# Kernel tuning notes

Measured on AMD Instinct MI355X. Metric: run time of the kernel, lower is better.

The kernel has to match this reference:

```python
import jax, jax.numpy as jnp
import numpy as np

B, S, F_IN, D, DFF, MEM, L, H = 32, 512, 64, 512, 2048, 1024, 3, 8
K_NEIGH = 3
TEMP = 1.0


def _pos_encoding(s, d):
    pos = np.arange(s, dtype=np.float64)[:, None]
    div = np.exp(np.arange(0, d, 2, dtype=np.float64) * (-np.log(10000.0) / d))
    pe = np.zeros((s, d), np.float32)
    pe[:, 0::2] = np.sin(pos * div)
    pe[:, 1::2] = np.cos(pos * div)
    return jnp.asarray(pe)


def _ln(x, g, b, eps=1e-5):
    m = x.mean(-1, keepdims=True)
    v = ((x - m) ** 2).mean(-1, keepdims=True)
    return (x - m) * jax.lax.rsqrt(v + eps) * g + b


def _mha(x, qkv_w, qkv_b, out_w, out_b):
    b, s, d = x.shape
    dh = d // H
    qkv = x @ qkv_w.T + qkv_b                      # (b,s,3d)
    q, k, v = jnp.split(qkv, 3, axis=-1)
    rs = lambda t: t.reshape(b, s, H, dh).transpose(0, 2, 1, 3)   # (b,h,s,dh)
    q, k, v = rs(q), rs(k), rs(v)
    scores = jnp.einsum('bhqd,bhkd->bhqk', q, k) / np.sqrt(dh).astype(np.float32)
    att = jax.nn.softmax(scores, axis=-1)
    o = jnp.einsum('bhqk,bhkd->bhqd', att, v).transpose(0, 2, 1, 3).reshape(b, s, d)
    return o @ out_w.T + out_b


def _construct_graph(x):
    # x: (B, S, F) -> adjacency (B, F, F) via kNN on rank-1 similarity (as in source)
    f = x.mean(axis=1)                                   # (B,F)
    n = jnp.linalg.norm(f, axis=1, keepdims=True)
    fn = f / jnp.maximum(n, 1e-12)                       # F.normalize over full vector
    sim = jnp.einsum('bi,bj->bij', fn, fn)               # (B,F,F)
    nf = f.shape[1]
    k = min(K_NEIGH, nf - 1)
    _, idx = jax.lax.top_k(sim, k + 1)                   # (B,F,k+1)
    idx = idx[..., 1:]                                   # drop top-1 (self under source's assumption)
    bidx = jnp.arange(f.shape[0])[:, None, None]
    ridx = jnp.arange(nf)[None, :, None]
    A = jnp.zeros((f.shape[0], nf, nf), x.dtype).at[bidx, ridx, idx].set(1.0)
    A = jnp.maximum(A, jnp.swapaxes(A, 1, 2))            # symmetrize
    di = jnp.arange(nf)
    return A.at[:, di, di].set(1.0)                      # fill_diagonal_(1)


def _gcn(x, A, w1, b1, w2, b2):
    deg = A.sum(2, keepdims=True)
    An = A / jnp.where(deg == 0, jnp.ones_like(deg), deg)
    xt = jnp.swapaxes(x, 1, 2)                           # (B,F,S)
    h = jax.nn.relu(jnp.einsum('bfg,bgh->bfh', An, xt @ w1.T + b1))
    h = jnp.einsum('bfg,bgh->bfh', An, h @ w2.T + b2)
    return jnp.swapaxes(h, 1, 2)                         # (B,S,F)


def _metg_forward(x, W_in, b_in, qkv_w, qkv_b, out_w, out_b, ln1_g, ln1_b,
                  ln2_g, ln2_b, ff1_w, ff1_b, ff2_w, ff2_b, memory,
                  fc1_w, fc1_b, fc2_w, fc2_b, gc1_w, gc1_b, gc2_w, gc2_b):
    # transformer branch
    h = x @ W_in.T + b_in                                # (B,S,D)
    h = h + _pos_encoding(h.shape[1], h.shape[2])
    for l in range(L):  # post-norm TransformerEncoderLayer, relu FFN, dropout=eval
        h = _ln(h + _mha(h, qkv_w[l], qkv_b[l], out_w[l], out_b[l]), ln1_g[l], ln1_b[l])
        ff = jax.nn.relu(h @ ff1_w[l].T + ff1_b[l]) @ ff2_w[l].T + ff2_b[l]
        h = _ln(h + ff, ln2_g[l], ln2_b[l])
    # memory module
    sims = (h @ memory.T) / TEMP                         # (B,S,MEM)
    attn = jax.nn.softmax(sims, axis=-1)
    upd = attn @ memory                                  # (B,S,D)
    # decoder
    cat = jnp.concatenate([h, upd], axis=-1)             # (B,S,2D)
    t_out = jax.nn.relu(cat @ fc1_w.T + fc1_b) @ fc2_w.T + fc2_b
    # GCN branch
    A = _construct_graph(x)
    g_out = _gcn(x, A, gc1_w, gc1_b, gc2_w, gc2_b)
    return t_out, g_out, attn


def setup_inputs() -> dict:
    key = jax.random.key(0)
    ks = jax.random.split(key, 12)
    w = lambda k, shape, s=0.02: jax.random.normal(k, shape, jnp.float32) * s
    return {
        'x': jax.random.normal(ks[0], (B, S, F_IN), jnp.float32),
        'W_in': w(ks[1], (D, F_IN)), 'b_in': jnp.zeros((D,), jnp.float32),
        'qkv_w': w(ks[2], (L, 3 * D, D)), 'qkv_b': jnp.zeros((L, 3 * D), jnp.float32),
        'out_w': w(ks[3], (L, D, D)), 'out_b': jnp.zeros((L, D), jnp.float32),
        'ln1_g': jnp.ones((L, D), jnp.float32), 'ln1_b': jnp.zeros((L, D), jnp.float32),
        'ln2_g': jnp.ones((L, D), jnp.float32), 'ln2_b': jnp.zeros((L, D), jnp.float32),
        'ff1_w': w(ks[4], (L, DFF, D)), 'ff1_b': jnp.zeros((L, DFF), jnp.float32),
        'ff2_w': w(ks[5], (L, D, DFF)), 'ff2_b': jnp.zeros((L, D), jnp.float32),
        'memory': w(ks[6], (MEM, D), 0.05),
        'fc1_w': w(ks[7], (D, 2 * D)), 'fc1_b': jnp.zeros((D,), jnp.float32),
        'fc2_w': w(ks[8], (F_IN, D)), 'fc2_b': jnp.zeros((F_IN,), jnp.float32),
        'gc1_w': w(ks[9], (D, S)), 'gc1_b': jnp.zeros((D,), jnp.float32),
        'gc2_w': w(ks[10], (S, D)), 'gc2_b': jnp.zeros((S,), jnp.float32),
    }


def reference(x, W_in, b_in, qkv_w, qkv_b, out_w, out_b, ln1_g, ln1_b,
              ln2_g, ln2_b, ff1_w, ff1_b, ff2_w, ff2_b, memory,
              fc1_w, fc1_b, fc2_w, fc2_b, gc1_w, gc1_b, gc2_w, gc2_b):
    return _metg_forward(x, W_in, b_in, qkv_w, qkv_b, out_w, out_b, ln1_g, ln1_b,
                         ln2_g, ln2_b, ff1_w, ff1_b, ff2_w, ff2_b, memory,
                         fc1_w, fc1_b, fc2_w, fc2_b, gc1_w, gc1_b, gc2_w, gc2_b)
```

## Files before the change

kernel.cpp:

```cpp
#include <hip/hip_runtime.h>
#include <hip/hip_bf16.h>
#include <math.h>


namespace {

typedef unsigned short ushort_t;
using bf16x8 = __attribute__((ext_vector_type(8))) __bf16;
using f32x4 = __attribute__((ext_vector_type(4))) float;
using ushort8 = __attribute__((ext_vector_type(8))) unsigned short;

constexpr int Mrows = 32 * 512;
constexpr size_t MB = 1048576;

__device__ __forceinline__ unsigned short f2bf(float f) {
  unsigned int u = __builtin_bit_cast(unsigned int, f);
  u += 0x7fffu + ((u >> 16) & 1u);
  return (unsigned short)(u >> 16);
}
__device__ __forceinline__ float bf2f(ushort_t u) {
  unsigned int v = ((unsigned int)u) << 16;
  return __builtin_bit_cast(float, v);
}

__device__ __forceinline__ void g2lds16(const void* g, void* l) {
  __builtin_amdgcn_global_load_lds(
      (const __attribute__((address_space(1))) unsigned int*)g,
      (__attribute__((address_space(3))) unsigned int*)l, 16, 0, 0);
}

template <bool RELU, bool BF16OUT>
__global__ __launch_bounds__(256) void gemm_bf16(const ushort_t* __restrict__ A,
                                                 const ushort_t* __restrict__ B,
                                                 const float* __restrict__ bias,
                                                 void* __restrict__ Cv,
                                                 int K, int lda, int ldc, int Nclip) {
  __shared__ __align__(16) ushort_t As[128 * 64];
  __shared__ __align__(16) ushort_t Bs[128 * 64];
  const int t = threadIdx.x;
  const int w = t >> 6, l = t & 63;
  const int m0 = blockIdx.x << 7, n0 = blockIdx.y << 7;
  const int srow8 = l >> 3;
  const int scol = ((l & 7) ^ srow8) << 3;
  const ushort_t* agp = A + (size_t)(m0 + w * 32 + srow8) * lda + scol;
  const ushort_t* bgp = B + (size_t)(n0 + w * 32 + srow8) * K + scol;
  ushort_t* alds = &As[(w * 32) * 64];
  ushort_t* blds = &Bs[(w * 32) * 64];
  const int wr = w >> 1, wc = w & 1;
  const int lr = l & 15, g = l >> 4;
  const int sw = (l & 7) << 4;
  f32x4 acc[4][4] = {};
  for (int kt = 0; kt < K; kt += 64) {
    __syncthreads();
#pragma unroll
    for (int i = 0; i < 4; ++i) {
      g2lds16(agp + (size_t)(i * 8) * lda + kt, alds + i * 8 * 64);
      g2lds16(bgp + (size_t)(i * 8) * K + kt, blds + i * 8 * 64);
    }
    __syncthreads();
#pragma unroll
    for (int ki = 0; ki < 2; ++ki) {
      bf16x8 af[4], bf[4];
      const int kb = (ki * 64 + g * 16) ^ sw;
#pragma unroll
      for (int mi = 0; mi < 4; ++mi)
        af[mi] = *(const bf16x8*)((const char*)As + (wr * 64 + mi * 16 + lr) * 128 + kb);
#pragma unroll
      for (int ni = 0; ni < 4; ++ni)
        bf[ni] = *(const bf16x8*)((const char*)Bs + (wc * 64 + ni * 16 + lr) * 128 + kb);
#pragma unroll
      for (int mi = 0; mi < 4; ++mi)
#pragma unroll
        for (int ni = 0; ni < 4; ++ni)
          acc[mi][ni] = __builtin_amdgcn_mfma_f32_16x16x32_bf16(af[mi], bf[ni],
                                                                acc[mi][ni], 0, 0, 0);
    }
  }
  float bb[4];
#pragma unroll
  for (int ni = 0; ni < 4; ++ni) {
    const int ci = n0 + wc * 64 + ni * 16 + lr;
    bb[ni] = (bias && ci < Nclip) ? bias[ci] : 0.f;
  }
  const int crow0 = m0 + wr * 64 + g * 4;
#pragma unroll
  for (int mi = 0; mi < 4; ++mi)
#pragma unroll
    for (int ni = 0; ni < 4; ++ni) {
      const int ci = n0 + wc * 64 + ni * 16 + lr;
      if (ci >= Nclip) continue;
#pragma unroll
      for (int v = 0; v < 4; ++v) {
        float val = acc[mi][ni][v] + bb[ni];
        if (RELU) val = fmaxf(val, 0.f);
        const size_t off = (size_t)(crow0 + mi * 16 + v) * ldc + ci;
        if (BF16OUT) ((ushort_t*)Cv)[off] = f2bf(val);
        else         ((float*)Cv)[off] = val;
      }
    }
}

__global__ __launch_bounds__(256) void flash_attn_mfma(const ushort_t* __restrict__ qkvb,
                                                       ushort_t* __restrict__ ctxb) {
  __shared__ __align__(16) ushort_t Qs[64 * 64];
  __shared__ __align__(16) ushort_t Ks[64 * 64];
  __shared__ __align__(16) ushort_t VT[64 * 64];
  __shared__ __align__(16) ushort_t Ps[64 * 64];
  const int qb = blockIdx.x, hh = blockIdx.y, b = blockIdx.z;
  const int t = threadIdx.x, w = t >> 6, l = t & 63;
  const int g = l >> 4, lr = l & 15, l7 = l & 7;
  const ushort_t* qkv0 = qkvb + (size_t)b * 512 * 1536 + hh * 64;
  {
    const int r8 = l >> 3;
    const int gcol = (l7 ^ r8) << 3;
#pragma unroll
    for (int i = 0; i < 2; ++i) {
      const int row = w * 16 + i * 8 + r8;
      g2lds16(qkv0 + (size_t)(qb * 64 + row) * 1536 + gcol, &Qs[(w * 16 + i * 8) * 64]);
    }
  }
  float mst = -INFINITY, lst = 0.f;
  f32x4 oacc[4] = {};
  const int vk0 = (t & 31) * 2;
  const int vdh0 = (t >> 5) * 8;
  for (int kt = 0; kt < 8; ++kt) {
    __syncthreads();
    {
      const int r8 = l >> 3;
      const int gcol = (l7 ^ r8) << 3;
#pragma unroll
      for (int i = 0; i < 2; ++i) {
        const int row = w * 16 + i * 8 + r8;
        g2lds16(qkv0 + 512 + (size_t)(kt * 64 + row) * 1536 + gcol,
                &Ks[(w * 16 + i * 8) * 64]);
      }
    }
    {
      const ushort_t* vp = qkv0 + 1024 + (size_t)(kt * 64 + vk0) * 1536 + vdh0;
      ushort8 v0 = *(const ushort8*)vp;
      ushort8 v1 = *(const ushort8*)(vp + 1536);
      const int slotbase = vk0 >> 3;
      const int inb = (vk0 & 7) * 2;
#pragma unroll
      for (int e = 0; e < 8; ++e) {
        const int dh = vdh0 + e;
        unsigned int word = (unsigned int)v0[e] | ((unsigned int)v1[e] << 16);
        *(unsigned int*)((char*)VT + dh * 128 + (((slotbase ^ (dh & 7)) << 4) + inb)) = word;
      }
    }
    __syncthreads();
    f32x4 sacc[4] = {};
#pragma unroll
    for (int ki = 0; ki < 2; ++ki) {
      const int sb = ((ki * 4 + g) ^ l7) << 4;
      bf16x8 qf = *(const bf16x8*)((const char*)Qs + (w * 16 + lr) * 128 + sb);
#pragma unroll
      for (int mi = 0; mi < 4; ++mi) {
        bf16x8 kf = *(const bf16x8*)((const char*)Ks + (mi * 16 + lr) * 128 + sb);
        sacc[mi] = __builtin_amdgcn_mfma_f32_16x16x32_bf16(kf, qf, sacc[mi], 0, 0, 0);
      }
    }
    float p[4][4];
    float cmax = -INFINITY;
#pragma unroll
    for (int mi = 0; mi < 4; ++mi)
#pragma unroll
      for (int v = 0; v < 4; ++v) {
        p[mi][v] = sacc[mi][v] * 0.125f;
        cmax = fmaxf(cmax, p[mi][v]);
      }
    cmax = fmaxf(cmax, __shfl_xor(cmax, 16));
    cmax = fmaxf(cmax, __shfl_xor(cmax, 32));
    const float mnew = fmaxf(mst, cmax);
    const float al = __expf(mst - mnew);
    float csum = 0.f;
#pragma unroll
    for (int mi = 0; mi < 4; ++mi)
#pragma unroll
      for (int v = 0; v < 4; ++v) {
        p[mi][v] = __expf(p[mi][v] - mnew);
        csum += p[mi][v];
      }
    csum += __shfl_xor(csum, 16);
    csum += __shfl_xor(csum, 32);
    lst = lst * al + csum;
    mst = mnew;
#pragma unroll
    for (int mi = 0; mi < 4; ++mi) oacc[mi] *= al;
    {
      char* pbase = (char*)Ps + (w * 16 + lr) * 128;
#pragma unroll
      for (int mi = 0; mi < 4; ++mi)
#pragma unroll
        for (int vp2 = 0; vp2 < 2; ++vp2) {
          const int klo = mi * 16 + g * 4 + vp2 * 2;
          unsigned int word = (unsigned int)f2bf(p[mi][vp2 * 2]) |
                              ((unsigned int)f2bf(p[mi][vp2 * 2 + 1]) << 16);
          *(unsigned int*)(pbase + (((klo >> 3) ^ l7) << 4) + (klo & 7) * 2) = word;
        }
    }
#pragma unroll
    for (int ki = 0; ki < 2; ++ki) {
      const int sb = ((ki * 4 + g) ^ l7) << 4;
      bf16x8 pf = *(const bf16x8*)((const char*)Ps + (w * 16 + lr) * 128 + sb);
#pragma unroll
      for (int mi = 0; mi < 4; ++mi) {
        bf16x8 vf = *(const bf16x8*)((const char*)VT + (mi * 16 + lr) * 128 + sb);
        oacc[mi] = __builtin_amdgcn_mfma_f32_16x16x32_bf16(vf, pf, oacc[mi], 0, 0, 0);
      }
    }
  }
  const float inv = 1.f / lst;
  ushort_t* op = ctxb + (size_t)(b * 512 + qb * 64 + w * 16 + lr) * 512 + hh * 64;
#pragma unroll
  for (int mi = 0; mi < 4; ++mi)
#pragma unroll
    for (int vp2 = 0; vp2 < 2; ++vp2) {
      const int dh = mi * 16 + g * 4 + vp2 * 2;
      unsigned int word = (unsigned int)f2bf(oacc[mi][vp2 * 2] * inv) |
                          ((unsigned int)f2bf(oacc[mi][vp2 * 2 + 1] * inv) << 16);
      *(unsigned int*)(op + dh) = word;
    }
}

#define OUTER16(ACC, A4, B4) do { \
  ACC[0][0] += (A4).x*(B4).x; ACC[0][1] += (A4).x*(B4).y; ACC[0][2] += (A4).x*(B4).z; ACC[0][3] += (A4).x*(B4).w; \
  ACC[1][0] += (A4).y*(B4).x; ACC[1][1] += (A4).y*(B4).y; ACC[1][2] += (A4).y*(B4).z; ACC[1][3] += (A4).y*(B4).w; \
  ACC[2][0] += (A4).z*(B4).x; ACC[2][1] += (A4).z*(B4).y; ACC[2][2] += (A4).z*(B4).z; ACC[2][3] += (A4).z*(B4).w; \
  ACC[3][0] += (A4).w*(B4).x; ACC[3][1] += (A4).w*(B4).y; ACC[3][2] += (A4).w*(B4).z; ACC[3][3] += (A4).w*(B4).w; \
} while (0)

__global__ __launch_bounds__(256) void win_pe_gemm(const float* __restrict__ A,
                                                   const float* __restrict__ Bm,
                                                   const float* __restrict__ bias,
                                                   const float* __restrict__ peb,
                                                   ushort_t* __restrict__ hbb) {
  __shared__ float As[16][68];
  __shared__ float Bs[16][68];
  const int t = threadIdx.x;
  const int m0 = blockIdx.x << 6;
  const int n0 = blockIdx.y << 6;
  const int r0 = (t >> 4) << 2;
  const int c0 = (t & 15) << 2;
  const int lm = t >> 2;
  const int lk4 = (t & 3) << 2;
  float acc[4][4] = {{0.f, 0.f, 0.f, 0.f}, {0.f, 0.f, 0.f, 0.f},
                     {0.f, 0.f, 0.f, 0.f}, {0.f, 0.f, 0.f, 0.f}};
  for (int kt = 0; kt < 64; kt += 16) {
    __syncthreads();
    float4 av = *reinterpret_cast<const float4*>(A + (size_t)(m0 + lm) * 64 + kt + lk4);
    As[lk4 + 0][lm] = av.x; As[lk4 + 1][lm] = av.y;
    As[lk4 + 2][lm] = av.z; As[lk4 + 3][lm] = av.w;
    float4 bv = *reinterpret_cast<const float4*>(Bm + (size_t)(n0 + lm) * 64 + kt + lk4);
    Bs[lk4 + 0][lm] = bv.x; Bs[lk4 + 1][lm] = bv.y;
    Bs[lk4 + 2][lm] = bv.z; Bs[lk4 + 3][lm] = bv.w;
    __syncthreads();
#pragma unroll
    for (int k = 0; k < 16; ++k) {
      float4 a4 = *reinterpret_cast<const float4*>(&As[k][r0]);
      float4 b4 = *reinterpret_cast<const float4*>(&Bs[k][c0]);
      OUTER16(acc, a4, b4);
    }
  }
  const float bb0 = bias[n0 + c0 + 0], bb1 = bias[n0 + c0 + 1];
  const float bb2 = bias[n0 + c0 + 2], bb3 = bias[n0 + c0 + 3];
#pragma unroll
  for (int i = 0; i < 4; ++i) {
    const int row = m0 + r0 + i;
    float4 p = *reinterpret_cast<const float4*>(peb + (size_t)(row & 511) * 512 + n0 + c0);
    ushort4 ob;
    ob.x = f2bf(acc[i][0] + bb0 + p.x);
    ob.y = f2bf(acc[i][1] + bb1 + p.y);
    ob.z = f2bf(acc[i][2] + bb2 + p.z);
    ob.w = f2bf(acc[i][3] + bb3 + p.w);
    *reinterpret_cast<ushort4*>(hbb + (size_t)row * 512 + n0 + c0) = ob;
  }
}

__global__ __launch_bounds__(256) void ln_wave(const ushort_t* __restrict__ hbi,
                                               const ushort_t* __restrict__ resb,
                                               const float* __restrict__ g,
                                               const float* __restrict__ bt,
                                               ushort_t* __restrict__ hbo, int hbs) {
  const int t = threadIdx.x;
  const size_t row = (size_t)blockIdx.x * 4 + (t >> 6);
  const int lane = t & 63;
  const size_t base = row * 512 + lane * 8;
  ushort8 hv = *reinterpret_cast<const ushort8*>(hbi + base);
  ushort8 rv = *reinterpret_cast<const ushort8*>(resb + base);
  float xs[8];
  float sum = 0.f;
#pragma unroll
  for (int i = 0; i < 8; ++i) { xs[i] = bf2f(hv[i]) + bf2f(rv[i]); sum += xs[i]; }
#pragma unroll
  for (int off = 1; off < 64; off <<= 1) sum += __shfl_xor(sum, off);
  const float mean = sum * (1.f / 512.f);
  float vs = 0.f;
#pragma unroll
  for (int i = 0; i < 8; ++i) { xs[i] -= mean; vs += xs[i] * xs[i]; }
#pragma unroll
  for (int off = 1; off < 64; off <<= 1) vs += __shfl_xor(vs, off);
  const float rstd = rsqrtf(vs * (1.f / 512.f) + 1e-5f);
  float4 g0 = *reinterpret_cast<const float4*>(g + lane * 8);
  float4 g1 = *reinterpret_cast<const float4*>(g + lane * 8 + 4);
  float4 b0 = *reinterpret_cast<const float4*>(bt + lane * 8);
  float4 b1 = *reinterpret_cast<const float4*>(bt + lane * 8 + 4);
  ushort8 o;
  o[0] = f2bf(xs[0] * rstd * g0.x + b0.x); o[1] = f2bf(xs[1] * rstd * g0.y + b0.y);
  o[2] = f2bf(xs[2] * rstd * g0.z + b0.z); o[3] = f2bf(xs[3] * rstd * g0.w + b0.w);
  o[4] = f2bf(xs[4] * rstd * g1.x + b1.x); o[5] = f2bf(xs[5] * rstd * g1.y + b1.y);
  o[6] = f2bf(xs[6] * rstd * g1.z + b1.z); o[7] = f2bf(xs[7] * rstd * g1.w + b1.w);
  *reinterpret_cast<ushort8*>(hbo + row * hbs + lane * 8) = o;
}

__global__ __launch_bounds__(256) void softmax_wave(const ushort_t* __restrict__ simsb,
                                                    float* __restrict__ attn,
                                                    ushort_t* __restrict__ attnb) {
  const int t = threadIdx.x;
  const size_t row = (size_t)blockIdx.x * 4 + (t >> 6);
  const int lane = t & 63;
  const size_t base = row * 1024 + lane * 16;
  ushort8 v0 = *reinterpret_cast<const ushort8*>(simsb + base);
  ushort8 v1 = *reinterpret_cast<const ushort8*>(simsb + base + 8);
  float xs[16];
  float mx = -INFINITY;
#pragma unroll
  for (int i = 0; i < 8; ++i) { xs[i] = bf2f(v0[i]); xs[i + 8] = bf2f(v1[i]); }
#pragma unroll
  for (int i = 0; i < 16; ++i) mx = fmaxf(mx, xs[i]);
#pragma unroll
  for (int off = 1; off < 64; off <<= 1) mx = fmaxf(mx, __shfl_xor(mx, off));
  float sum = 0.f;
#pragma unroll
  for (int i = 0; i < 16; ++i) { xs[i] = __expf(xs[i] - mx); sum += xs[i]; }
#pragma unroll
  for (int off = 1; off < 64; off <<= 1) sum += __shfl_xor(sum, off);
  const float inv = 1.f / sum;
  ushort8 o0, o1;
#pragma unroll
  for (int i = 0; i < 16; ++i) xs[i] *= inv;
#pragma unroll
  for (int i = 0; i < 4; ++i) {
    float4 f = make_float4(xs[4 * i], xs[4 * i + 1], xs[4 * i + 2], xs[4 * i + 3]);
    *reinterpret_cast<float4*>(attn + base + 4 * i) = f;
  }
#pragma unroll
  for (int i = 0; i < 8; ++i) { o0[i] = f2bf(xs[i]); o1[i] = f2bf(xs[i + 8]); }
  *reinterpret_cast<ushort8*>(attnb + base) = o0;
  *reinterpret_cast<ushort8*>(attnb + base + 8) = o1;
}

__global__ void pe_kernel(float* __restrict__ pe) {
  const int s = blockIdx.x, i = threadIdx.x;
  double div = exp((double)(2 * i) * (-log(10000.0) / 512.0));
  double a = (double)s * div;
  pe[s * 512 + 2 * i] = (float)sin(a);
  pe[s * 512 + 2 * i + 1] = (float)cos(a);
}

__global__ __launch_bounds__(256) void cvt_all(
    const float* __restrict__ qkvw, const float* __restrict__ outw,
    const float* __restrict__ ff1w, const float* __restrict__ ff2w,
    const float* __restrict__ memw, const float* __restrict__ fc1w,
    const float* __restrict__ gc1w, const float* __restrict__ gc2w,
    const float* __restrict__ fc2w,
    ushort_t* qkvb, ushort_t* outb, ushort_t* ff1b, ushort_t* ff2b,
    ushort_t* memb, ushort_t* fc1b, ushort_t* gc1b, ushort_t* gc2b,
    ushort_t* fc2p) {
  const int gidx = blockIdx.x * 256 + threadIdx.x;
  if (gidx >= 2768896) return;
  if (gidx >= 2752512) {
    const int off = gidx - 2752512;
    ushort4 o = {0, 0, 0, 0};
    if (off < 8192) {
      float4 v = reinterpret_cast<const float4*>(fc2w)[off];
      o.x = f2bf(v.x); o.y = f2bf(v.y); o.z = f2bf(v.z); o.w = f2bf(v.w);
    }
    reinterpret_cast<ushort4*>(fc2p)[off] = o;
    return;
  }
  const float* s; ushort_t* d; int off;
  if (gidx < 589824)        { s = qkvw; d = qkvb; off = gidx; }
  else if (gidx < 786432)   { s = outw; d = outb; off = gidx - 589824; }
  else if (gidx < 1572864)  { s = ff1w; d = ff1b; off = gidx - 786432; }
  else if (gidx < 2359296)  { s = ff2w; d = ff2b; off = gidx - 1572864; }
  else if (gidx < 2490368)  { s = memw; d = memb; off = gidx - 2359296; }
  else if (gidx < 2621440)  { s = fc1w; d = fc1b; off = gidx - 2490368; }
  else if (gidx < 2686976)  { s = gc1w; d = gc1b; off = gidx - 2621440; }
  else                      { s = gc2w; d = gc2b; off = gidx - 2686976; }
  float4 v = reinterpret_cast<const float4*>(s)[off];
  ushort4 o;
  o.x = f2bf(v.x); o.y = f2bf(v.y); o.z = f2bf(v.z); o.w = f2bf(v.w);
  reinterpret_cast<ushort4*>(d)[off] = o;
}

__global__ __launch_bounds__(256) void transpose_cvt(const float* __restrict__ in,
                                                     ushort_t* __restrict__ out) {
  const int g = blockIdx.x * 256 + threadIdx.x;
  const int r = g >> 9, c = g & 511;
  out[(size_t)c * 1024 + r] = f2bf(in[g]);
}

__global__ __launch_bounds__(256) void transpose_x_bf16(const float* __restrict__ x,
                                                        ushort_t* __restrict__ xtb) {
  __shared__ float Ls[64][65];
  const int sc = blockIdx.x, b = blockIdx.y;
  const int t = threadIdx.x;
  const int f = t & 63, sr = t >> 6;
#pragma unroll
  for (int j = 0; j < 16; ++j) {
    const int s = sr + 4 * j;
    Ls[s][f] = x[((size_t)(b * 512 + sc * 64 + s)) * 64 + f];
  }
  __syncthreads();
#pragma unroll
  for (int j = 0; j < 16; ++j) {
    const int fr = sr * 16 + j;
    xtb[((size_t)b * 64 + fr) * 512 + sc * 64 + f] = f2bf(Ls[f][fr]);
  }
}

__global__ __launch_bounds__(256) void fmean2(const float* __restrict__ x,
                                              float* __restrict__ fn) {
  __shared__ float part[4][64];
  const int b = blockIdx.x, t = threadIdx.x;
  const int f = t & 63, sg = t >> 6;
  float acc = 0.f;
  const float* xp = x + ((size_t)b * 512 + sg) * 64 + f;
  for (int s = sg; s < 512; s += 4, xp += 256) acc += *xp;
  part[sg][f] = acc;
  __syncthreads();
  if (t < 64) {
    float m = (part[0][t] + part[1][t] + part[2][t] + part[3][t]) * (1.f / 512.f);
    float ss = m * m;
#pragma unroll
    for (int off = 32; off; off >>= 1) ss += __shfl_xor(ss, off);
    float n = fmaxf(sqrtf(ss), 1e-12f);
    fn[b * 64 + t] = m / n;
  }
}

__global__ __launch_bounds__(256) void graph_kernel2(const float* __restrict__ fn,
                                                     float* __restrict__ An) {
  __shared__ float fv[64];
  __shared__ float Am[64][65];
  const int b = blockIdx.x, t = threadIdx.x;
  const int i = t >> 2, g = t & 3;
  if (t < 64) fv[t] = fn[b * 64 + t];
#pragma unroll
  for (int j = 0; j < 16; ++j) Am[i][g * 16 + j] = 0.f;
  __syncthreads();
  const float fi = fv[i];
  unsigned int mask = 0;
  int sel[4];
  for (int r = 0; r < 4; ++r) {
    float best = -INFINITY;
    int bi = 1 << 30;
    for (int j = 0; j < 16; ++j) {
      if (mask & (1u << j)) continue;
      float v = fi * fv[g * 16 + j];
      if (v > best) { best = v; bi = g * 16 + j; }
    }
#pragma unroll
    for (int off = 1; off < 4; off <<= 1) {
      float ov = __shfl_xor(best, off);
      int oi = __shfl_xor(bi, off);
      if (ov > best || (ov == best && oi < bi)) { best = ov; bi = oi; }
    }
    sel[r] = bi;
    if ((bi >> 4) == g) mask |= 1u << (bi & 15);
  }
  if (g == 0) { Am[i][sel[1]] = 1.f; Am[i][sel[2]] = 1.f; Am[i][sel[3]] = 1.f; }
  __syncthreads();
  float vals[16];
  float deg = 0.f;
#pragma unroll
  for (int j0 = 0; j0 < 16; ++j0) {
    const int j = g * 16 + j0;
    float v = (j == i) ? 1.f : fmaxf(Am[i][j], Am[j][i]);
    vals[j0] = v;
    deg += v;
  }
#pragma unroll
  for (int off = 1; off < 4; off <<= 1) deg += __shfl_xor(deg, off);
  const float inv = 1.f / deg;
  float* out = An + ((size_t)b * 64 + i) * 64 + g * 16;
#pragma unroll
  for (int j0 = 0; j0 < 16; ++j0) out[j0] = vals[j0] * inv;
}

template <bool RELU, bool STORE_T>
__global__ __launch_bounds__(256) void bmm_an(const float* __restrict__ An,
                                              const float* __restrict__ X,
                                              float* __restrict__ Y,
                                              ushort_t* __restrict__ Yb) {
  __shared__ float Ag[64][68];
  __shared__ float Xs[64][68];
  const int nc = blockIdx.x << 6;
  const int b = blockIdx.y;
  const int t = threadIdx.x;
  {
    const int i = t >> 2, g0 = (t & 3) << 4;
    const float* ap = An + ((size_t)b * 64 + i) * 64 + g0;
#pragma unroll
    for (int j = 0; j < 16; ++j) Ag[g0 + j][i] = ap[j];
  }
  {
    const int g = t >> 2, n4 = (t & 3) << 4;
    const float* xp = X + ((size_t)b * 64 + g) * 512 + nc + n4;
#pragma unroll
    for (int j = 0; j < 4; ++j)
      *reinterpret_cast<float4*>(&Xs[g][n4 + 4 * j]) =
          *reinterpret_cast<const float4*>(xp + 4 * j);
  }
  __syncthreads();
  const int r0 = (t >> 4) << 2, c0 = (t & 15) << 2;
  float acc[4][4] = {{0.f, 0.f, 0.f, 0.f}, {0.f, 0.f, 0.f, 0.f},
                     {0.f, 0.f, 0.f, 0.f}, {0.f, 0.f, 0.f, 0.f}};
#pragma unroll 8
  for (int g = 0; g < 64; ++g) {
    float4 a4 = *reinterpret_cast<const float4*>(&Ag[g][r0]);
    float4 x4 = *reinterpret_cast<const float4*>(&Xs[g][c0]);
    OUTER16(acc, a4, x4);
  }
  if (!STORE_T) {
#pragma unroll
    for (int i = 0; i < 4; ++i) {
      float4 o = make_float4(acc[i][0], acc[i][1], acc[i][2], acc[i][3]);
      if (RELU) {
        o.x = fmaxf(o.x, 0.f); o.y = fmaxf(o.y, 0.f);
        o.z = fmaxf(o.z, 0.f); o.w = fmaxf(o.w, 0.f);
      }
      ushort4 ob;
      ob.x = f2bf(o.x); ob.y = f2bf(o.y); ob.z = f2bf(o.z); ob.w = f2bf(o.w);
      *reinterpret_cast<ushort4*>(Yb + ((size_t)b * 64 + r0 + i) * 512 + nc + c0) = ob;
    }
  } else {
#pragma unroll
    for (int j = 0; j < 4; ++j) {
      float4 o = make_float4(acc[0][j], acc[1][j], acc[2][j], acc[3][j]);
      *reinterpret_cast<float4*>(Y + ((size_t)b * 512 + nc + c0 + j) * 64 + r0) = o;
    }
  }
}

}

extern "C" void kernel_launch(void* const* d_in, const int* in_sizes, int n_in,
                              void* d_out, int out_size, void* d_ws, size_t ws_size,
                              hipStream_t stream) {
  const float* x     = (const float*)d_in[0];
  const float* W_in  = (const float*)d_in[1];
  const float* b_in  = (const float*)d_in[2];
  const float* qkv_w = (const float*)d_in[3];
  const float* qkv_b = (const float*)d_in[4];
  const float* out_w = (const float*)d_in[5];
  const float* out_b = (const float*)d_in[6];
  const float* ln1_g = (const float*)d_in[7];
  const float* ln1_b = (const float*)d_in[8];
  const float* ln2_g = (const float*)d_in[9];
  const float* ln2_b = (const float*)d_in[10];
  const float* ff1_w = (const float*)d_in[11];
  const float* ff1_b = (const float*)d_in[12];
  const float* ff2_w = (const float*)d_in[13];
  const float* ff2_b = (const float*)d_in[14];
  const float* memw  = (const float*)d_in[15];
  const float* fc1_w = (const float*)d_in[16];
  const float* fc1_b = (const float*)d_in[17];
  const float* fc2_w = (const float*)d_in[18];
  const float* fc2_b = (const float*)d_in[19];
  const float* gc1_w = (const float*)d_in[20];
  const float* gc1_b = (const float*)d_in[21];
  const float* gc2_w = (const float*)d_in[22];
  const float* gc2_b = (const float*)d_in[23];

  char* wsb = (char*)d_ws;
  ushort_t* hb     = (ushort_t*)(wsb + 0);
  ushort_t* ctxb   = (ushort_t*)(wsb + 16 * MB);
  ushort_t* resb   = (ushort_t*)(wsb + 32 * MB);
  char*     U1     = wsb + 48 * MB;
  float*    pe     = (float*)(wsb + 144 * MB);
  ushort_t* qkv_wb = (ushort_t*)(wsb + 146 * MB);
  ushort_t* out_wb = (ushort_t*)(wsb + 151 * MB);
  ushort_t* ff1_wb = (ushort_t*)(wsb + 153 * MB);
  ushort_t* ff2_wb = (ushort_t*)(wsb + 160 * MB);
  ushort_t* mem_b  = (ushort_t*)(wsb + 166 * MB);
  ushort_t* memT_b = (ushort_t*)(wsb + 167 * MB);
  ushort_t* fc1_wb = (ushort_t*)(wsb + 168 * MB);
  ushort_t* gc1_wb = (ushort_t*)(wsb + 169 * MB);
  ushort_t* gc2_wb = (ushort_t*)(wsb + 169 * MB + 524288);
  ushort_t* fc2_wp = (ushort_t*)(wsb + 170 * MB);
  float*    fn     = (float*)(wsb + 171 * MB);
  float*    An     = (float*)(wsb + 172 * MB);

  ushort_t* qkvb    = (ushort_t*)U1;
  ushort_t* midb    = (ushort_t*)U1;
  ushort_t* catb    = (ushort_t*)U1;
  ushort_t* simsb   = (ushort_t*)(U1 + 32 * MB);
  ushort_t* attnb   = (ushort_t*)(U1 + 64 * MB);
  ushort_t* fc1outb = (ushort_t*)(U1 + 64 * MB);
  ushort_t* xtb  = (ushort_t*)U1;
  float*    t1   = (float*)(U1 + 2 * MB);
  ushort_t* h1b  = (ushort_t*)(U1 + 6 * MB);
  float*    t2   = (float*)(U1 + 8 * MB);

  float* t_out = (float*)d_out;
  float* g_out = t_out + 1048576;
  float* attn  = g_out + 1048576;

  hipLaunchKernelGGL(cvt_all, dim3(10816), dim3(256), 0, stream,
                     qkv_w, out_w, ff1_w, ff2_w, memw, fc1_w, gc1_w, gc2_w, fc2_w,
                     qkv_wb, out_wb, ff1_wb, ff2_wb, mem_b, fc1_wb, gc1_wb, gc2_wb,
                     fc2_wp);
  hipLaunchKernelGGL(transpose_cvt, dim3(2048), dim3(256), 0, stream, memw, memT_b);
  hipLaunchKernelGGL(pe_kernel, dim3(512), dim3(256), 0, stream, pe);

  hipLaunchKernelGGL(win_pe_gemm, dim3(256, 8), dim3(256), 0, stream,
                     x, W_in, b_in, pe, hb);

  for (int l = 0; l < 3; ++l) {
    hipLaunchKernelGGL((gemm_bf16<false, true>), dim3(128, 12), dim3(256), 0, stream,
                       hb, qkv_wb + (size_t)l * 786432, qkv_b + l * 1536, qkvb,
                       512, 512, 1536, 1536);
    hipLaunchKernelGGL(flash_attn_mfma, dim3(8, 8, 32), dim3(256), 0, stream, qkvb, ctxb);
    hipLaunchKernelGGL((gemm_bf16<false, true>), dim3(128, 4), dim3(256), 0, stream,
                       ctxb, out_wb + (size_t)l * 262144, out_b + l * 512, resb,
                       512, 512, 512, 512);
    hipLaunchKernelGGL(ln_wave, dim3(Mrows / 4), dim3(256), 0, stream,
                       hb, resb, ln1_g + l * 512, ln1_b + l * 512, hb, 512);
    hipLaunchKernelGGL((gemm_bf16<true, true>), dim3(128, 16), dim3(256), 0, stream,
                       hb, ff1_wb + (size_t)l * 1048576, ff1_b + l * 2048, midb,
                       512, 512, 2048, 2048);
    hipLaunchKernelGGL((gemm_bf16<false, true>), dim3(128, 4), dim3(256), 0, stream,
                       midb, ff2_wb + (size_t)l * 1048576, ff2_b + l * 512, resb,
                       2048, 2048, 512, 512);
    if (l < 2) {
      hipLaunchKernelGGL(ln_wave, dim3(Mrows / 4), dim3(256), 0, stream,
                         hb, resb, ln2_g + l * 512, ln2_b + l * 512, hb, 512);
    } else {
      hipLaunchKernelGGL(ln_wave, dim3(Mrows / 4), dim3(256), 0, stream,
                         hb, resb, ln2_g + l * 512, ln2_b + l * 512, catb, 1024);
    }
  }

  hipLaunchKernelGGL((gemm_bf16<false, true>), dim3(128, 8), dim3(256), 0, stream,
                     catb, mem_b, (const float*)nullptr, simsb,
                     512, 1024, 1024, 1024);
  hipLaunchKernelGGL(softmax_wave, dim3(Mrows / 4), dim3(256), 0, stream,
                     simsb, attn, attnb);
  hipLaunchKernelGGL((gemm_bf16<false, true>), dim3(128, 4), dim3(256), 0, stream,
                     attnb, memT_b, (const float*)nullptr, catb + 512,
                     1024, 1024, 1024, 512);
  hipLaunchKernelGGL((gemm_bf16<true, true>), dim3(128, 4), dim3(256), 0, stream,
                     catb, fc1_wb, fc1_b, fc1outb, 1024, 1024, 512, 512);
  hipLaunchKernelGGL((gemm_bf16<false, false>), dim3(128, 1), dim3(256), 0, stream,
                     fc1outb, fc2_wp, fc2_b, t_out, 512, 512, 64, 64);

  hipLaunchKernelGGL(fmean2, dim3(32), dim3(256), 0, stream, x, fn);
  hipLaunchKernelGGL(graph_kernel2, dim3(32), dim3(256), 0, stream, fn, An);
  hipLaunchKernelGGL(transpose_x_bf16, dim3(8, 32), dim3(256), 0, stream, x, xtb);
  hipLaunchKernelGGL((gemm_bf16<false, false>), dim3(16, 4), dim3(256), 0, stream,
                     xtb, gc1_wb, gc1_b, t1, 512, 512, 512, 512);
  hipLaunchKernelGGL((bmm_an<true, false>), dim3(8, 32), dim3(256), 0, stream,
                     An, t1, (float*)nullptr, h1b);
  hipLaunchKernelGGL((gemm_bf16<false, false>), dim3(16, 4), dim3(256), 0, stream,
                     h1b, gc2_wb, gc2_b, t2, 512, 512, 512, 512);
  hipLaunchKernelGGL((bmm_an<false, true>), dim3(8, 32), dim3(256), 0, stream,
                     An, t2, g_out, (ushort_t*)nullptr);
}
```

Before: 934.8 us.

## Add 256x256 double-buffered bf16 GEMM for QKV, FF1 and memory-sim GEMMs

Introduces a 512-thread GEMM kernel with 256x256 output tiles and double-buffered LDS loads via global_load_lds. It is used for the wide QKV, FF1 and memory-similarity GEMMs. Larger tiles raise arithmetic intensity and reduce global traffic per FLOP, and the double buffer overlaps loads with MFMA work. The costs are a 128KB LDS footprint and heavy register use from 32 accumulators, which may limit occupancy, and the smaller grids (e.g. 384 blocks) may fill the CUs less evenly.

Result: faster. 900.9 us (-3.6%).

```diff
diff --git a/kernel.cpp b/kernel.cpp
--- a/kernel.cpp
+++ b/kernel.cpp
@@ -27,6 +27,97 @@
   __builtin_amdgcn_global_load_lds(
       (const __attribute__((address_space(1))) unsigned int*)g,
       (__attribute__((address_space(3))) unsigned int*)l, 16, 0, 0);
+}
+
+template <bool RELU, bool BF16OUT>
+__global__ __launch_bounds__(512, 2) void gemm256(const ushort_t* __restrict__ A,
+                                                  const ushort_t* __restrict__ B,
+                                                  const float* __restrict__ bias,
+                                                  void* __restrict__ Cv,
+                                                  int K, int lda, int ldc) {
+  __shared__ __align__(16) ushort_t As[2][256 * 64];
+  __shared__ __align__(16) ushort_t Bs[2][256 * 64];
+  const int t = threadIdx.x;
+  const int w = t >> 6, l = t & 63;
+  const int m0 = blockIdx.x << 8, n0 = blockIdx.y << 8;
+  const int srow8 = l >> 3;
+  const int scol = ((l & 7) ^ srow8) << 3;
+  const ushort_t* agp = A + (size_t)(m0 + w * 32 + srow8) * lda + scol;
+  const ushort_t* bgp = B + (size_t)(n0 + w * 32 + srow8) * K + scol;
+  const int wr = w >> 2, wcn = w & 3;
+  const int lr = l & 15, g = l >> 4;
+  const int sw = (l & 7) << 4;
+  const int nt = K >> 6;
+  f32x4 acc[8][4] = {};
+#pragma unroll
+  for (int i = 0; i < 4; ++i) {
+    g2lds16(agp + (size_t)(i * 8) * lda, &As[0][(w * 32 + i * 8) * 64]);
+    g2lds16(bgp + (size_t)(i * 8) * K, &Bs[0][(w * 32 + i * 8) * 64]);
+  }
+#pragma unroll
+  for (int i = 0; i < 4; ++i) {
+    g2lds16(agp + (size_t)(i * 8) * lda + 64, &As[1][(w * 32 + i * 8) * 64]);
+    g2lds16(bgp + (size_t)(i * 8) * K + 64, &Bs[1][(w * 32 + i * 8) * 64]);
+  }
+  for (int j = 0; j < nt; ++j) {
+    const int c = j & 1;
+    asm volatile("s_waitcnt vmcnt(8)" ::: "memory");
+    __builtin_amdgcn_s_barrier();
+    asm volatile("" ::: "memory");
+    const char* abase = (const char*)&As[c][0];
+    const char* bbase = (const char*)&Bs[c][0];
+#pragma unroll
+    for (int ki = 0; ki < 2; ++ki) {
+      const int kb = (ki * 64 + g * 16) ^ sw;
+      bf16x8 af[8], bfr[4];
+#pragma unroll
+      for (int mi = 0; mi < 8; ++mi)
+        af[mi] = *(const bf16x8*)(abase + (wr * 128 + mi * 16 + lr) * 128 + kb);
+#pragma unroll
+      for (int ni = 0; ni < 4; ++ni)
+        bfr[ni] = *(const bf16x8*)(bbase + (wcn * 64 + ni * 16 + lr) * 128 + kb);
+      __builtin_amdgcn_s_setprio(1);
+#pragma unroll
+      for (int mi = 0; mi < 8; ++mi)
+#pragma unroll
+        for (int ni = 0; ni < 4; ++ni)
+          acc[mi][ni] = __builtin_amdgcn_mfma_f32_16x16x32_bf16(af[mi], bfr[ni],
+                                                                acc[mi][ni], 0, 0, 0);
+      __builtin_amdgcn_s_setprio(0);
+    }
+    asm volatile("s_waitcnt lgkmcnt(0)" ::: "memory");
+    __builtin_amdgcn_s_barrier();
+    asm volatile("" ::: "memory");
+    if (j + 2 < nt) {
+      const size_t ko = (size_t)(j + 2) * 64;
+#pragma unroll
+      for (int i = 0; i < 4; ++i) {
+        g2lds16(agp + (size_t)(i * 8) * lda + ko, &As[c][(w * 32 + i * 8) * 64]);
+        g2lds16(bgp + (size_t)(i * 8) * K + ko, &Bs[c][(w * 32 + i * 8) * 64]);
+      }
+    }
+  }
+  float bb[4];
+#pragma unroll
+  for (int ni = 0; ni < 4; ++ni) {
+    const int ci = n0 + wcn * 64 + ni * 16 + lr;
+    bb[ni] = bias ? bias[ci] : 0.f;
+  }
+  const int crow0 = m0 + wr * 128 + g * 4;
+#pragma unroll
+  for (int mi = 0; mi < 8; ++mi)
+#pragma unroll
+    for (int ni = 0; ni < 4; ++ni) {
+      const int ci = n0 + wcn * 64 + ni * 16 + lr;
+#pragma unroll
+      for (int v = 0; v < 4; ++v) {
+        float val = acc[mi][ni][v] + bb[ni];
+        if (RELU) val = fmaxf(val, 0.f);
+        const size_t off = (size_t)(crow0 + mi * 16 + v) * ldc + ci;
+        if (BF16OUT) ((ushort_t*)Cv)[off] = f2bf(val);
+        else         ((float*)Cv)[off] = val;
+      }
+    }
 }
 
 template <bool RELU, bool BF16OUT>
@@ -619,18 +710,18 @@
                      x, W_in, b_in, pe, hb);
 
   for (int l = 0; l < 3; ++l) {
-    hipLaunchKernelGGL((gemm_bf16<false, true>), dim3(128, 12), dim3(256), 0, stream,
+    hipLaunchKernelGGL((gemm256<false, true>), dim3(64, 6), dim3(512), 0, stream,
                        hb, qkv_wb + (size_t)l * 786432, qkv_b + l * 1536, qkvb,
-                       512, 512, 1536, 1536);
+                       512, 512, 1536);
     hipLaunchKernelGGL(flash_attn_mfma, dim3(8, 8, 32), dim3(256), 0, stream, qkvb, ctxb);
     hipLaunchKernelGGL((gemm_bf16<false, true>), dim3(128, 4), dim3(256), 0, stream,
                        ctxb, out_wb + (size_t)l * 262144, out_b + l * 512, resb,
                        512, 512, 512, 512);
     hipLaunchKernelGGL(ln_wave, dim3(Mrows / 4), dim3(256), 0, stream,
                        hb, resb, ln1_g + l * 512, ln1_b + l * 512, hb, 512);
-    hipLaunchKernelGGL((gemm_bf16<true, true>), dim3(128, 16), dim3(256), 0, stream,
+    hipLaunchKernelGGL((gemm256<true, true>), dim3(64, 8), dim3(512), 0, stream,
                        hb, ff1_wb + (size_t)l * 1048576, ff1_b + l * 2048, midb,
-                       512, 512, 2048, 2048);
+                       512, 512, 2048);
     hipLaunchKernelGGL((gemm_bf16<false, true>), dim3(128, 4), dim3(256), 0, stream,
                        midb, ff2_wb + (size_t)l * 1048576, ff2_b + l * 512, resb,
                        2048, 2048, 512, 512);
@@ -643,9 +734,9 @@
     }
   }
 
-  hipLaunchKernelGGL((gemm_bf16<false, true>), dim3(128, 8), dim3(256), 0, stream,
+  hipLaunchKernelGGL((gemm256<false, true>), dim3(64, 4), dim3(512), 0, stream,
                      catb, mem_b, (const float*)nullptr, simsb,
-                     512, 1024, 1024, 1024);
+                     512, 1024, 1024);
   hipLaunchKernelGGL(softmax_wave, dim3(Mrows / 4), dim3(256), 0, stream,
                      simsb, attn, attnb);
   hipLaunchKernelGGL((gemm_bf16<false, true>), dim3(128, 4), dim3(256), 0, stream,
```
